# Kernel tuning notes

Measured on AMD Instinct MI355X. Metric: run time of the kernel, lower is better.

Reference implementation:

```python
import jax, jax.numpy as jnp
import numpy as np
import math, itertools

DIM = 384; KEY_DIM = 16; HEADS = 8; ATTN_RATIO = 4; RES = 28
RES2 = math.ceil(RES / 2)            # 14
NH_KD = KEY_DIM * HEADS              # 128
D = ATTN_RATIO * KEY_DIM             # 64
DH = D * HEADS                       # 512
N = RES * RES                        # 784
N2 = RES2 * RES2                     # 196
OUT_DIM = DIM
SCALE = KEY_DIM ** -0.5
BATCH = 64


def build_bias_idxs():
    stride = math.ceil(RES / RES2)
    offsets = {}
    idxs = []
    for p1 in itertools.product(range(RES2), repeat=2):
        for p2 in itertools.product(range(RES), repeat=2):
            off = (abs(p1[0] * stride - p2[0]), abs(p1[1] * stride - p2[1]))
            if off not in offsets:
                offsets[off] = len(offsets)
            idxs.append(offsets[off])
    return np.asarray(idxs, dtype=np.int32), len(offsets)


def dwconv(x, w, b, stride):
    # depthwise 3x3, padding 1; x: (B,C,H,W), w: (C,1,3,3)
    y = jax.lax.conv_general_dilated(
        x, w, (stride, stride), ((1, 1), (1, 1)),
        dimension_numbers=("NCHW", "OIHW", "NCHW"),
        feature_group_count=x.shape[1])
    return y + b[None, :, None, None]


def conv1x1(x, w, b):
    return jnp.einsum("bchw,oc->bohw", x, w) + b[None, :, None, None]


def bn(x, s, o):
    # inference-mode BatchNorm folded to per-channel scale/offset
    return x * s[None, :, None, None] + o[None, :, None, None]


def setup_inputs() -> dict:
    key = jax.random.key(0)
    ks = jax.random.split(key, 25)
    def rn(k, shape, sc=0.05):
        return jax.random.normal(k, shape, jnp.float32) * sc
    idxs, n_off = build_bias_idxs()
    return dict(
        x=jax.random.normal(ks[0], (BATCH, DIM, RES, RES), jnp.float32),
        ql_w=rn(ks[1], (DIM, 1, 3, 3)), ql_b=rn(ks[2], (DIM,)),
        qp_w=rn(ks[3], (NH_KD, DIM)), qp_b=rn(ks[4], (NH_KD,)),
        qp_s=1.0 + rn(ks[5], (NH_KD,)), qp_o=rn(ks[6], (NH_KD,)),
        k_w=rn(ks[7], (NH_KD, DIM)), k_b=rn(ks[8], (NH_KD,)),
        k_s=1.0 + rn(ks[9], (NH_KD,)), k_o=rn(ks[10], (NH_KD,)),
        v_w=rn(ks[11], (DH, DIM)), v_b=rn(ks[12], (DH,)),
        v_s=1.0 + rn(ks[13], (DH,)), v_o=rn(ks[14], (DH,)),
        vl_w=rn(ks[15], (DH, 1, 3, 3)), vl_b=rn(ks[16], (DH,)),
        vl_s=1.0 + rn(ks[17], (DH,)), vl_o=rn(ks[18], (DH,)),
        p_w=rn(ks[19], (OUT_DIM, DH)), p_b=rn(ks[20], (OUT_DIM,)),
        p_s=1.0 + rn(ks[21], (OUT_DIM,)), p_o=rn(ks[22], (OUT_DIM,)),
        ab=rn(ks[23], (HEADS, n_off)),
        bias_idxs=jnp.asarray(idxs),
    )


def reference(x, ql_w, ql_b, qp_w, qp_b, qp_s, qp_o,
              k_w, k_b, k_s, k_o, v_w, v_b, v_s, v_o,
              vl_w, vl_b, vl_s, vl_o, p_w, p_b, p_s, p_o,
              ab, bias_idxs):
    B = x.shape[0]
    # LGQuery: depthwise stride-2 conv + stride-2 avg-pool(k=1), then 1x1 conv + BN
    local_q = dwconv(x, ql_w, ql_b, 2)
    pool_q = x[:, :, ::2, ::2]               # AvgPool2d(1, 2, 0)
    q = bn(conv1x1(local_q + pool_q, qp_w, qp_b), qp_s, qp_o)
    q = q.reshape(B, HEADS, KEY_DIM, N2).transpose(0, 1, 3, 2)   # (B,H,N2,kd)

    k = bn(conv1x1(x, k_w, k_b), k_s, k_o).reshape(B, HEADS, KEY_DIM, N)  # (B,H,kd,N)

    v = bn(conv1x1(x, v_w, v_b), v_s, v_o)   # (B,DH,RES,RES)
    v_local = bn(dwconv(v, vl_w, vl_b, 2), vl_s, vl_o)           # (B,DH,RES2,RES2)
    v = v.reshape(B, HEADS, D, N).transpose(0, 1, 3, 2)          # (B,H,N,d)

    bias = ab[:, bias_idxs].reshape(HEADS, N2, N)                # gathered rel-pos bias
    attn = jnp.einsum("bhqc,bhck->bhqk", q, k) * SCALE + bias[None]
    attn = jax.nn.softmax(attn, axis=-1)

    out = jnp.einsum("bhqk,bhkd->bhqd", attn, v).transpose(0, 1, 3, 2)
    out = out.reshape(B, DH, RES2, RES2) + v_local
    out = bn(conv1x1(jax.nn.gelu(out, approximate=False), p_w, p_b), p_s, p_o)
    return out
```

## Files before the change

### kernel.cpp

```cpp
#include <hip/hip_runtime.h>
#include <math.h>

#define BATCH   64
#define DIMC    384
#define KEY_DIM 16
#define HEADS   8
#define DD      64
#define DH      512
#define NH_KD   128
#define RES     28
#define RES2    14
#define NN      784
#define NN2     196
#define OUT_DIM 384
#define SCALE   0.25f
#define XPAD    896
#define QPAD    256
#define KPAD    832
#define XSP     796

typedef __attribute__((ext_vector_type(8))) short bf16x8;
typedef __attribute__((ext_vector_type(4))) float f32x4;

#define MFMA32(a, b, c) __builtin_amdgcn_mfma_f32_16x16x32_bf16(a, b, c, 0, 0, 0)
#define SWZ(row, bcol) ((row) * 64 + ((bcol) ^ ((((row) >> 1) & 3) << 4)))

__device__ inline short f2bf(float f) {
    unsigned u = __float_as_uint(f);
    unsigned r = (u + 0x7fff + ((u >> 16) & 1)) >> 16;
    return (short)r;
}
__device__ inline float bf2f(short h) {
    return __uint_as_float(((unsigned)(unsigned short)h) << 16);
}
__device__ __forceinline__ unsigned cvt_pk_bf16(float a, float b) {
    unsigned r;
    asm("v_cvt_pk_bf16_f32 %0, %1, %2" : "=v"(r) : "v"(a), "v"(b));
    return r;
}
__device__ __forceinline__ void gload16(const void* g, void* l) {
    __builtin_amdgcn_global_load_lds((const __attribute__((address_space(1))) void*)g,
                                     (__attribute__((address_space(3))) void*)l, 16, 0, 0);
}

#define O_XT_HI    0u
#define O_QINT_HI  44040192u
#define O_QT       88080384u
#define O_KT       96468992u
#define O_V        123731968u
#define O_VLOCAL   178257920u
#define O_BIASB    203948032u
#define O_W_HI     206557184u
#define O_W_LO     207540224u
#define O_ATTNT    0u
#define O_GT_HI    25690112u

__global__ __launch_bounds__(256)
void xprep_kernel(const float* __restrict__ x, const float* __restrict__ ql_w,
                  const float* __restrict__ ql_b, short* __restrict__ xT,
                  short* __restrict__ qinT) {
    __shared__ short xs[32 * XSP];
    const int cg = blockIdx.x, b = blockIdx.y;
    const int t = threadIdx.x;
    const float* xb = x + ((size_t)b * DIMC + cg * 32) * NN;

    {
        const int c = t >> 3, sub = t & 7;
        const float* xc = xb + (size_t)c * NN;
        short* dst = xs + c * XSP;
        #pragma unroll 5
        for (int p4 = sub; p4 < 196; p4 += 8) {
            float4 v = *(const float4*)(xc + p4 * 4);
            uint2 pk = {cvt_pk_bf16(v.x, v.y), cvt_pk_bf16(v.z, v.w)};
            *(uint2*)(dst + p4 * 4) = pk;
        }
    }
    __syncthreads();

    {
        const int c_l = t & 31;
        const int ng  = t >> 5;
        const short* src = xs + c_l * XSP;
        short* dstb = xT + (size_t)b * XPAD * DIMC + cg * 32 + c_l;
        for (int n = ng; n < NN; n += 8)
            dstb[(size_t)n * DIMC] = src[n];
        for (int n = NN + ng; n < XPAD; n += 8)
            dstb[(size_t)n * DIMC] = 0;
    }

    {
        const int c_l = t & 31;
        const int ng  = t >> 5;
        const int c = cg * 32 + c_l;
        const short* xc = xs + c_l * XSP;
        const float* w = ql_w + c * 9;
        const float w0 = w[0], w1 = w[1], w2 = w[2], w3 = w[3], w4 = w[4],
                    w5 = w[5], w6 = w[6], w7 = w[7], w8 = w[8];
        const float bias = ql_b[c];
        short* qdst = qinT + (size_t)b * QPAD * DIMC + c;
        for (int n2 = ng; n2 < NN2; n2 += 8) {
            int i = n2 / RES2, j = n2 % RES2;
            int r0 = 2 * i - 1, c0 = 2 * j - 1;
            float acc = bias;
            if (r0 >= 0) {
                if (c0 >= 0)       acc += bf2f(xc[r0 * RES + c0])     * w0;
                                   acc += bf2f(xc[r0 * RES + c0 + 1]) * w1;
                if (c0 + 2 < RES)  acc += bf2f(xc[r0 * RES + c0 + 2]) * w2;
            }
            {
                if (c0 >= 0)       acc += bf2f(xc[(r0 + 1) * RES + c0])     * w3;
                                   acc += bf2f(xc[(r0 + 1) * RES + c0 + 1]) * w4;
                if (c0 + 2 < RES)  acc += bf2f(xc[(r0 + 1) * RES + c0 + 2]) * w5;
            }
            if (r0 + 2 < RES) {
                if (c0 >= 0)       acc += bf2f(xc[(r0 + 2) * RES + c0])     * w6;
                                   acc += bf2f(xc[(r0 + 2) * RES + c0 + 1]) * w7;
                if (c0 + 2 < RES)  acc += bf2f(xc[(r0 + 2) * RES + c0 + 2]) * w8;
            }
            acc += bf2f(xc[(2 * i) * RES + 2 * j]);
            qdst[(size_t)n2 * DIMC] = f2bf(acc);
        }
        for (int n2 = NN2 + ng; n2 < QPAD; n2 += 8)
            qdst[(size_t)n2 * DIMC] = 0;
    }
}

__global__ void wsplit_kernel(const float* __restrict__ w0, const float* __restrict__ w1,
                              const float* __restrict__ w2, const float* __restrict__ w3,
                              short* __restrict__ hi, short* __restrict__ lo) {
    int i = blockIdx.x * 256 + threadIdx.x;
    if (i >= 491520) return;
    const float* src; int j = i;
    if (j < 49152) src = w0;
    else if (j < 98304) { src = w1; j -= 49152; }
    else if (j < 294912) { src = w2; j -= 98304; }
    else { src = w3; j -= 294912; }
    float v = src[j];
    short h = f2bf(v);
    hi[i] = h;
    lo[i] = f2bf(v - bf2f(h));
}

template<bool WLO, bool SWAP>
__global__ __launch_bounds__(256)
void gemm_split_kernel(const short* __restrict__ wgt_hi, const short* __restrict__ wgt_lo,
                       const short* __restrict__ act,
                       const float* __restrict__ bias, const float* __restrict__ s,
                       const float* __restrict__ off,
                       float* __restrict__ out_f, short* __restrict__ out_b,
                       int mode, int C, int Nn, int Npad, int NPADo, float pscale,
                       int NXn, int NYo, int O) {
    constexpr int NT = 2 + (WLO ? 1 : 0);
    constexpr int STRIDE = NT * 8192;
    constexpr int OFF_A = 0, OFF_B = 8192, OFF_WL = 16384;
    __shared__ __align__(1024) char LDS[2 * STRIDE];

    const int bid = blockIdx.x;
    const int xcd = bid & 7;
    const int g   = bid >> 3;
    const int ot  = g % NYo;
    const int pp  = (g / NYo) * 8 + xcd;
    const int nt  = pp % NXn;
    const int b   = pp / NXn;
    const int n0 = nt * 128, o0 = ot * 128;

    const int t = threadIdx.x;
    const int lane = t & 63, wid = t >> 6;
    const int wm = wid & 1, wn = wid >> 1;
    const int lr = lane & 15, kg = lane >> 4;

    const short* Ahi = SWAP ? act : wgt_hi;
    const short* Bhi = SWAP ? wgt_hi : act;

    f32x4 acc[4][4];
    #pragma unroll
    for (int m = 0; m < 4; ++m)
        #pragma unroll
        for (int n = 0; n < 4; ++n)
            acc[m][n] = (f32x4){0.f, 0.f, 0.f, 0.f};

    const int ccol = (lane & 3) * 16;
    const int r0   = wid * 32 + (lane >> 2);

    auto STAGE = [&](int buf, int k0) {
        char* base = LDS + buf * STRIDE;
        #pragma unroll
        for (int c = 0; c < 2; ++c) {
            int r = r0 + c * 16;
            int bcs = ccol ^ (((r >> 1) & 3) << 4);
            size_t aRow = SWAP ? ((size_t)b * Npad + n0 + r) : (size_t)(o0 + r);
            size_t bRow = SWAP ? (size_t)(o0 + r) : ((size_t)b * Npad + n0 + r);
            char* ldsc = base + wid * 2048 + c * 1024;
            gload16((const char*)Ahi + (aRow * C + k0) * 2 + bcs, ldsc + OFF_A);
            gload16((const char*)Bhi + (bRow * C + k0) * 2 + bcs, ldsc + OFF_B);
            if constexpr (WLO)
                gload16((const char*)wgt_lo + ((size_t)(o0 + r) * C + k0) * 2 + bcs, ldsc + OFF_WL);
        }
    };

    STAGE(0, 0);
    int cur = 0;
    __syncthreads();

    for (int k0 = 0;; k0 += 32) {
        const bool hasNext = (k0 + 32 < C);
        if (hasNext) STAGE(cur ^ 1, k0 + 32);

        char* cb = LDS + cur * STRIDE;
        bf16x8 ah[4], wlm[4];
        #pragma unroll
        for (int m = 0; m < 4; ++m) {
            int row = wm * 64 + m * 16 + lr;
            ah[m] = *(const bf16x8*)(cb + OFF_A + SWZ(row, kg * 16));
            if constexpr (WLO) if (!SWAP) wlm[m] = *(const bf16x8*)(cb + OFF_WL + SWZ(row, kg * 16));
        }
        #pragma unroll
        for (int nf = 0; nf < 4; ++nf) {
            int row = wn * 64 + nf * 16 + lr;
            bf16x8 bh = *(const bf16x8*)(cb + OFF_B + SWZ(row, kg * 16));
            bf16x8 blw;
            if constexpr (WLO) if (SWAP) blw = *(const bf16x8*)(cb + OFF_WL + SWZ(row, kg * 16));
            #pragma unroll
            for (int m = 0; m < 4; ++m) {
                acc[m][nf] = MFMA32(ah[m], bh, acc[m][nf]);
                if constexpr (WLO) {
                    if (SWAP) acc[m][nf] = MFMA32(ah[m], blw, acc[m][nf]);
                    else      acc[m][nf] = MFMA32(wlm[m], bh, acc[m][nf]);
                }
            }
        }
        if (!hasNext) break;
        __syncthreads();
        cur ^= 1;
    }

    if (mode == 2) {
        #pragma unroll
        for (int m = 0; m < 4; ++m) {
            #pragma unroll
            for (int nf = 0; nf < 4; ++nf) {
                int col = n0 + wn * 64 + nf * 16 + lr;
                if (col >= NPADo) continue;
                int hh = (o0 + wm * 64 + m * 16) >> 4;
                bool nok = (col < Nn);
                float v[4];
                #pragma unroll
                for (int r = 0; r < 4; ++r) {
                    int row = o0 + wm * 64 + m * 16 + kg * 4 + r;
                    float a = s[row];
                    v[r] = nok ? (acc[m][nf][r] * a + (bias[row] * a + off[row])) * pscale : 0.f;
                }
                unsigned h01 = cvt_pk_bf16(v[0], v[1]);
                unsigned h23 = cvt_pk_bf16(v[2], v[3]);
                float l0 = v[0] - __uint_as_float(h01 << 16);
                float l1 = v[1] - __uint_as_float(h01 & 0xffff0000u);
                float l2 = v[2] - __uint_as_float(h23 << 16);
                float l3 = v[3] - __uint_as_float(h23 & 0xffff0000u);
                uint2 hst = {h01, h23};
                uint2 lst = {cvt_pk_bf16(l0, l1), cvt_pk_bf16(l2, l3)};
                size_t base = ((size_t)(b * 8 + hh) * NPADo + col) * 32 + kg * 4;
                *(uint2*)(out_b + base)      = hst;
                *(uint2*)(out_b + base + 16) = lst;
            }
        }
    } else {
        #pragma unroll
        for (int nf = 0; nf < 4; ++nf) {
            int col_d = o0 + wn * 64 + nf * 16 + lr;
            float a = s[col_d];
            float badd = bias[col_d] * a + off[col_d];
            #pragma unroll
            for (int m = 0; m < 4; ++m) {
                int rown = n0 + wm * 64 + m * 16 + kg * 4;
                float v0 = acc[m][nf][0] * a + badd;
                float v1 = acc[m][nf][1] * a + badd;
                float v2 = acc[m][nf][2] * a + badd;
                float v3 = acc[m][nf][3] * a + badd;
                if (mode == 0) {
                    if (rown < Nn) {
                        float4 vv = {v0, v1, v2, v3};
                        *(float4*)(out_f + ((size_t)b * O + col_d) * Nn + rown) = vv;
                    }
                } else {
                    if (rown + 3 < NPADo) {
                        uint2 st = {cvt_pk_bf16(v0, v1), cvt_pk_bf16(v2, v3)};
                        *(uint2*)(out_b + ((size_t)b * O + col_d) * NPADo + rown) = st;
                    }
                }
            }
        }
    }
}

__global__ void vlocal_kernel(const short* __restrict__ v,
                              const float* __restrict__ vl_w, const float* __restrict__ vl_b,
                              const float* __restrict__ vl_s, const float* __restrict__ vl_o,
                              float* __restrict__ vlocal) {
    int c = blockIdx.x, b = blockIdx.y, n2 = threadIdx.x;
    if (n2 >= NN2) return;
    int i = n2 / RES2, j = n2 % RES2;
    const size_t base = ((size_t)b * DH + c) * KPAD;
    const float* w = vl_w + c * 9;
    float acc = vl_b[c];
    #pragma unroll
    for (int di = 0; di < 3; ++di) {
        int r = 2 * i + di - 1;
        if (r < 0 || r >= RES) continue;
        #pragma unroll
        for (int dj = 0; dj < 3; ++dj) {
            int cc = 2 * j + dj - 1;
            if (cc < 0 || cc >= RES) continue;
            acc += bf2f(v[base + r * RES + cc]) * w[di * 3 + dj];
        }
    }
    vlocal[((size_t)b * DH + c) * NN2 + n2] = acc * vl_s[c] + vl_o[c];
}

__global__ void biasB_expand_kernel(const float* __restrict__ ab, const int* __restrict__ bidx,
                                    short* __restrict__ biasB, int n_off) {
    int i = blockIdx.x * 256 + threadIdx.x;
    int h = blockIdx.y;
    if (i >= NN2 * KPAD) return;
    int q = i / KPAD, key = i - q * KPAD;
    short v = 0;
    if (key < NN) v = f2bf(ab[h * n_off + bidx[q * NN + key]]);
    biasB[(size_t)h * NN2 * KPAD + i] = v;
}

__global__ __launch_bounds__(512, 4)
void attn_mfma9_kernel(const short* __restrict__ QT, const short* __restrict__ KT,
                       const short* __restrict__ V, const short* __restrict__ biasB,
                       float* __restrict__ outT) {
    __shared__ __align__(1024) char LDS[2 * 12288 + 8 * 4096];

    const int t = threadIdx.x;
    const int bid = blockIdx.x;
    const int h = bid & 7;
    const int b = bid >> 3;

    const int lane = t & 63, wid = t >> 6;
    const int lr = lane & 15, kg = lane >> 4;
    const int wq0 = wid * 32;

    bf16x8 qb1[2], qb2[2];
    const short* bb[2];
    #pragma unroll
    for (int qf = 0; qf < 2; ++qf) {
        int qg = wq0 + qf * 16 + lr;
        const short* qrow = QT + ((size_t)(b * 8 + h) * QPAD + qg) * 32;
        qb1[qf] = *(const bf16x8*)(qrow + (kg & 1) * 8);
        qb2[qf] = (bf16x8){0, 0, 0, 0, 0, 0, 0, 0};
        if (kg < 2) qb2[qf] = *(const bf16x8*)(qrow + 16 + kg * 8);
        int qs = (qg < NN2) ? qg : (NN2 - 1);
        bb[qf] = biasB + ((size_t)h * NN2 + qs) * KPAD;
    }

    const short* kbase = KT + (size_t)(b * 8 + h) * KPAD * 32;
    const short* vbase = V + ((size_t)b * DH + h * DD) * KPAD;

    f32x4 acc[2][4];
    #pragma unroll
    for (int qf = 0; qf < 2; ++qf)
        #pragma unroll
        for (int nt = 0; nt < 4; ++nt)
            acc[qf][nt] = (f32x4){0.f, 0.f, 0.f, 0.f};
    float sacc[2] = {0.f, 0.f};
    char* PsW = LDS + 24576 + wid * 4096;
    const int swz = (lr & 7) << 4;

    auto STAGE = [&](int buf, int tile) {
        const int k0 = tile * 64;
        char* base = LDS + buf * 12288;
        #pragma unroll
        for (int ci = 0; ci < 2; ++ci) {
            if (ci == 1 && wid >= 4) continue;
            int chunk = (ci == 0) ? wid : wid + 8;
            if (chunk < 4) {
                int row = chunk * 16 + (lane >> 2);
                int pcol = (lane & 3) ^ ((row >> 1) & 3);
                gload16((const char*)(kbase + (size_t)(k0 + row) * 32) + pcol * 16,
                        base + chunk * 1024);
            } else {
                int vrow = (chunk - 4) * 8 + (lane >> 3);
                int pcol = (lane & 7) ^ (vrow & 7);
                gload16((const char*)(vbase + (size_t)vrow * KPAD + k0) + pcol * 16,
                        base + 4096 + (chunk - 4) * 1024);
            }
        }
    };

    auto COMPUTE = [&](int buf, int tile) {
        const int k0 = tile * 64;
        char* cb = LDS + buf * 12288;
        short4 b4[2][4];
        #pragma unroll
        for (int qf = 0; qf < 2; ++qf)
            #pragma unroll
            for (int nt = 0; nt < 4; ++nt)
                b4[qf][nt] = *(const short4*)(bb[qf] + k0 + nt * 16 + kg * 4);

        #pragma unroll
        for (int qf = 0; qf < 2; ++qf) {
            f32x4 sc[4];
            __builtin_amdgcn_s_setprio(1);
            #pragma unroll
            for (int nt = 0; nt < 4; ++nt) {
                int row = nt * 16 + lr;
                bf16x8 ka = *(const bf16x8*)(cb + row * 64 + ((kg ^ ((row >> 1) & 3)) * 16));
                sc[nt] = (f32x4){0.f, 0.f, 0.f, 0.f};
                sc[nt] = MFMA32(ka, qb1[qf], sc[nt]);
                sc[nt] = MFMA32(ka, qb2[qf], sc[nt]);
            }
            __builtin_amdgcn_s_setprio(0);

            char* Psw = PsW + qf * 2048;
            #pragma unroll
            for (int nt = 0; nt < 4; ++nt) {
                int keyb = k0 + nt * 16 + kg * 4;
                bool kvalid = keyb < NN;
                float pv[4];
                #pragma unroll
                for (int r = 0; r < 4; ++r) {
                    float sv = sc[nt][r] + bf2f(((const short*)&b4[qf][nt])[r]);
                    pv[r] = kvalid ? __expf(sv) : 0.f;
                    sacc[qf] += pv[r];
                }
                uint2 pk2 = {cvt_pk_bf16(pv[0], pv[1]), cvt_pk_bf16(pv[2], pv[3])};
                *(uint2*)(Psw + lr * 128 + ((nt * 32 + kg * 8) ^ swz)) = pk2;
            }
        }

        #pragma unroll
        for (int ks = 0; ks < 2; ++ks) {
            bf16x8 vf[4];
            #pragma unroll
            for (int nt = 0; nt < 4; ++nt) {
                int row = nt * 16 + lr;
                int pk_ = ks * 4 + kg;
                vf[nt] = *(const bf16x8*)(cb + 4096 + row * 128 + ((pk_ ^ (row & 7)) * 16));
            }
            #pragma unroll
            for (int qf = 0; qf < 2; ++qf) {
                bf16x8 pa = *(const bf16x8*)(PsW + qf * 2048 + lr * 128
                                             + ((ks * 64 + kg * 16) ^ swz));
                __builtin_amdgcn_s_setprio(1);
                #pragma unroll
                for (int nt = 0; nt < 4; ++nt)
                    acc[qf][nt] = MFMA32(pa, vf[nt], acc[qf][nt]);
                __builtin_amdgcn_s_setprio(0);
            }
        }
    };

    STAGE(0, 0);
    int cur = 0;
    __syncthreads();
    #pragma unroll 1
    for (int tile = 0; tile < 13; ++tile) {
        if (tile + 1 < 13) STAGE(cur ^ 1, tile + 1);
        COMPUTE(cur, tile);
        __syncthreads();
        cur ^= 1;
    }

    #pragma unroll
    for (int qf = 0; qf < 2; ++qf) {
        float sv = sacc[qf];
        sv += __shfl_xor(sv, 16, 64);
        sv += __shfl_xor(sv, 32, 64);
        #pragma unroll
        for (int r = 0; r < 4; ++r) {
            int qrow_ = wq0 + qf * 16 + kg * 4 + r;
            if (qrow_ >= NN2) continue;
            float inv = 1.f / __shfl(sv, kg * 4 + r, 64);
            #pragma unroll
            for (int nt = 0; nt < 4; ++nt) {
                int d = nt * 16 + lr;
                outT[((size_t)b * NN2 + qrow_) * DH + h * DD + d] = acc[qf][nt][r] * inv;
            }
        }
    }
}

__global__ void gelu_addT_kernel(const float* __restrict__ aT, const float* __restrict__ vloc,
                                 short* __restrict__ g_hi) {
    __shared__ float tile[32][33];
    int ntb = blockIdx.x * 32, ctb = blockIdx.y * 32, b = blockIdx.z;
    int tn = threadIdx.x & 31, tc4 = threadIdx.x >> 5;
    #pragma unroll
    for (int i = 0; i < 4; ++i) {
        int c = tc4 + i * 8;
        int n = ntb + tn;
        tile[c][tn] = (n < NN2) ? vloc[((size_t)b * DH + ctb + c) * NN2 + n] : 0.f;
    }
    __syncthreads();
    int tc = threadIdx.x & 31, tn4 = threadIdx.x >> 5;
    #pragma unroll
    for (int i = 0; i < 4; ++i) {
        int n = ntb + tn4 + i * 8;
        float g = 0.f;
        if (n < NN2) {
            float sum = aT[((size_t)b * NN2 + n) * DH + ctb + tc] + tile[tc][tn4 + i * 8];
            g = 0.5f * sum * (1.f + erff(sum * 0.70710678118654752440f));
        }
        g_hi[((size_t)b * QPAD + n) * DH + ctb + tc] = f2bf(g);
    }
}

extern "C" void kernel_launch(void* const* d_in, const int* in_sizes, int n_in,
                              void* d_out, int out_size, void* d_ws, size_t ws_size,
                              hipStream_t stream) {
    const float* x     = (const float*)d_in[0];
    const float* ql_w  = (const float*)d_in[1];
    const float* ql_b  = (const float*)d_in[2];
    const float* qp_w  = (const float*)d_in[3];
    const float* qp_b  = (const float*)d_in[4];
    const float* qp_s  = (const float*)d_in[5];
    const float* qp_o  = (const float*)d_in[6];
    const float* k_w   = (const float*)d_in[7];
    const float* k_b   = (const float*)d_in[8];
    const float* k_s   = (const float*)d_in[9];
    const float* k_o   = (const float*)d_in[10];
    const float* v_w   = (const float*)d_in[11];
    const float* v_b   = (const float*)d_in[12];
    const float* v_s   = (const float*)d_in[13];
    const float* v_o   = (const float*)d_in[14];
    const float* vl_w  = (const float*)d_in[15];
    const float* vl_b  = (const float*)d_in[16];
    const float* vl_s  = (const float*)d_in[17];
    const float* vl_o  = (const float*)d_in[18];
    const float* p_w   = (const float*)d_in[19];
    const float* p_b   = (const float*)d_in[20];
    const float* p_s   = (const float*)d_in[21];
    const float* p_o   = (const float*)d_in[22];
    const float* ab    = (const float*)d_in[23];
    const int*   bidx  = (const int*)d_in[24];
    float* out = (float*)d_out;
    int n_off = in_sizes[23] / HEADS;

    char* ws = (char*)d_ws;
    short* qinT_h = (short*)(ws + O_QINT_HI);
    short* xT_h   = (short*)(ws + O_XT_HI);
    short* QT     = (short*)(ws + O_QT);
    short* KT     = (short*)(ws + O_KT);
    short* Vb     = (short*)(ws + O_V);
    float* vlocal = (float*)(ws + O_VLOCAL);
    short* biasB  = (short*)(ws + O_BIASB);
    short* w_h    = (short*)(ws + O_W_HI);
    short* w_l    = (short*)(ws + O_W_LO);
    float* attnT  = (float*)(ws + O_ATTNT);
    short* gT_h   = (short*)(ws + O_GT_HI);

    xprep_kernel<<<dim3(DIMC / 32, BATCH), 256, 0, stream>>>(x, ql_w, ql_b, xT_h, qinT_h);
    wsplit_kernel<<<dim3(1920), 256, 0, stream>>>(qp_w, k_w, v_w, p_w, w_h, w_l);
    gemm_split_kernel<false, false><<<dim3(128), 256, 0, stream>>>(
        w_h + 0, nullptr, qinT_h, qp_b, qp_s, qp_o,
        nullptr, QT, 2, DIMC, NN2, QPAD, QPAD, SCALE, 2, 1, 128);
    gemm_split_kernel<false, false><<<dim3(448), 256, 0, stream>>>(
        w_h + 49152, nullptr, xT_h, k_b, k_s, k_o,
        nullptr, KT, 2, DIMC, NN, XPAD, KPAD, 1.0f, 7, 1, 128);
    gemm_split_kernel<false, true><<<dim3(1792), 256, 0, stream>>>(
        w_h + 98304, nullptr, xT_h, v_b, v_s, v_o,
        nullptr, Vb, 1, DIMC, NN, XPAD, KPAD, 1.0f, 7, 4, 512);
    vlocal_kernel<<<dim3(DH, BATCH), 256, 0, stream>>>(Vb, vl_w, vl_b, vl_s, vl_o, vlocal);
    biasB_expand_kernel<<<dim3((NN2 * KPAD + 255) / 256, HEADS), 256, 0, stream>>>(ab, bidx, biasB, n_off);
    attn_mfma9_kernel<<<dim3(HEADS * BATCH), 512, 0, stream>>>(QT, KT, Vb, biasB, attnT);
    gelu_addT_kernel<<<dim3(QPAD / 32, DH / 32, BATCH), 256, 0, stream>>>(attnT, vlocal, gT_h);
    gemm_split_kernel<true, true><<<dim3(384), 256, 0, stream>>>(
        w_h + 294912, w_l + 294912, gT_h, p_b, p_s, p_o,
        out, nullptr, 0, DH, NN2, QPAD, 0, 1.0f, 2, 3, 384);
}
```

Baseline: 274.3 us.

## Fuse vlocal add and GELU into attention epilogue, use exp2 softmax

Attention now adds the transposed v_local and applies exact GELU in its epilogue, writing bf16 directly for the projection GEMM. This removes the separate gelu_addT kernel and the fp32 attention intermediate. vlocal is rewritten to produce a token-major layout via an LDS transpose. log2(e) is folded into the Q scale and bias so the softmax uses exp2f. The final projection drops the hi/lo weight split, trading some precision for fewer MFMA passes.

```diff
diff --git a/kernel.cpp b/kernel.cpp
--- a/kernel.cpp
+++ b/kernel.cpp
@@ -14,6 +14,7 @@
 #define NN2     196
 #define OUT_DIM 384
 #define SCALE   0.25f
+#define LOG2E   1.44269504088896340736f
 #define XPAD    896
 #define QPAD    256
 #define KPAD    832
@@ -48,11 +49,10 @@
 #define O_QT       88080384u
 #define O_KT       96468992u
 #define O_V        123731968u
-#define O_VLOCAL   178257920u
+#define O_VLT      178257920u
 #define O_BIASB    203948032u
 #define O_W_HI     206557184u
 #define O_W_LO     207540224u
-#define O_ATTNT    0u
 #define O_GT_HI    25690112u
 
 __global__ __launch_bounds__(256)
@@ -292,28 +292,50 @@
     }
 }
 
-__global__ void vlocal_kernel(const short* __restrict__ v,
-                              const float* __restrict__ vl_w, const float* __restrict__ vl_b,
-                              const float* __restrict__ vl_s, const float* __restrict__ vl_o,
-                              float* __restrict__ vlocal) {
-    int c = blockIdx.x, b = blockIdx.y, n2 = threadIdx.x;
-    if (n2 >= NN2) return;
-    int i = n2 / RES2, j = n2 % RES2;
-    const size_t base = ((size_t)b * DH + c) * KPAD;
-    const float* w = vl_w + c * 9;
-    float acc = vl_b[c];
-    #pragma unroll
-    for (int di = 0; di < 3; ++di) {
-        int r = 2 * i + di - 1;
-        if (r < 0 || r >= RES) continue;
-        #pragma unroll
-        for (int dj = 0; dj < 3; ++dj) {
-            int cc = 2 * j + dj - 1;
-            if (cc < 0 || cc >= RES) continue;
-            acc += bf2f(v[base + r * RES + cc]) * w[di * 3 + dj];
-        }
-    }
-    vlocal[((size_t)b * DH + c) * NN2 + n2] = acc * vl_s[c] + vl_o[c];
+__global__ __launch_bounds__(256)
+void vlocalT_kernel(const short* __restrict__ v,
+                    const float* __restrict__ vl_w, const float* __restrict__ vl_b,
+                    const float* __restrict__ vl_s, const float* __restrict__ vl_o,
+                    float* __restrict__ vlT) {
+    __shared__ float tile[32][201];
+    const int cg = blockIdx.x, b = blockIdx.y;
+    const int t = threadIdx.x;
+    {
+        const int c_l = t >> 3, nsub = t & 7;
+        const int c = cg * 32 + c_l;
+        const size_t base = ((size_t)b * DH + c) * KPAD;
+        const float* w = vl_w + c * 9;
+        const float w0 = w[0], w1 = w[1], w2 = w[2], w3 = w[3], w4 = w[4],
+                    w5 = w[5], w6 = w[6], w7 = w[7], w8 = w[8];
+        const float bias = vl_b[c], sc = vl_s[c], of = vl_o[c];
+        for (int n2 = nsub; n2 < NN2; n2 += 8) {
+            int i = n2 / RES2, j = n2 % RES2;
+            int r0 = 2 * i - 1, c0 = 2 * j - 1;
+            float acc = bias;
+            if (r0 >= 0) {
+                if (c0 >= 0)       acc += bf2f(v[base + r0 * RES + c0])     * w0;
+                                   acc += bf2f(v[base + r0 * RES + c0 + 1]) * w1;
+                if (c0 + 2 < RES)  acc += bf2f(v[base + r0 * RES + c0 + 2]) * w2;
+            }
+            {
+                if (c0 >= 0)       acc += bf2f(v[base + (r0 + 1) * RES + c0])     * w3;
+                                   acc += bf2f(v[base + (r0 + 1) * RES + c0 + 1]) * w4;
+                if (c0 + 2 < RES)  acc += bf2f(v[base + (r0 + 1) * RES + c0 + 2]) * w5;
+            }
+            if (r0 + 2 < RES) {
+                if (c0 >= 0)       acc += bf2f(v[base + (r0 + 2) * RES + c0])     * w6;
+                                   acc += bf2f(v[base + (r0 + 2) * RES + c0 + 1]) * w7;
+                if (c0 + 2 < RES)  acc += bf2f(v[base + (r0 + 2) * RES + c0 + 2]) * w8;
+            }
+            tile[c_l][n2] = acc * sc + of;
+        }
+    }
+    __syncthreads();
+    {
+        const int c_l = t & 31, ng = t >> 5;
+        for (int n2 = ng; n2 < NN2; n2 += 8)
+            vlT[((size_t)b * NN2 + n2) * DH + cg * 32 + c_l] = tile[c_l][n2];
+    }
 }
 
 __global__ void biasB_expand_kernel(const float* __restrict__ ab, const int* __restrict__ bidx,
@@ -323,14 +345,14 @@
     if (i >= NN2 * KPAD) return;
     int q = i / KPAD, key = i - q * KPAD;
     short v = 0;
-    if (key < NN) v = f2bf(ab[h * n_off + bidx[q * NN + key]]);
+    if (key < NN) v = f2bf(ab[h * n_off + bidx[q * NN + key]] * LOG2E);
     biasB[(size_t)h * NN2 * KPAD + i] = v;
 }
 
 __global__ __launch_bounds__(512, 4)
-void attn_mfma9_kernel(const short* __restrict__ QT, const short* __restrict__ KT,
-                       const short* __restrict__ V, const short* __restrict__ biasB,
-                       float* __restrict__ outT) {
+void attn_mfma10_kernel(const short* __restrict__ QT, const short* __restrict__ KT,
+                        const short* __restrict__ V, const short* __restrict__ biasB,
+                        const float* __restrict__ vlT, short* __restrict__ gT) {
     __shared__ __align__(1024) char LDS[2 * 12288 + 8 * 4096];
 
     const int t = threadIdx.x;
@@ -422,7 +444,7 @@
                 #pragma unroll
                 for (int r = 0; r < 4; ++r) {
                     float sv = sc[nt][r] + bf2f(((const short*)&b4[qf][nt])[r]);
-                    pv[r] = kvalid ? __expf(sv) : 0.f;
+                    pv[r] = kvalid ? exp2f(sv) : 0.f;
                     sacc[qf] += pv[r];
                 }
                 uint2 pk2 = {cvt_pk_bf16(pv[0], pv[1]), cvt_pk_bf16(pv[2], pv[3])};
@@ -473,37 +495,16 @@
             int qrow_ = wq0 + qf * 16 + kg * 4 + r;
             if (qrow_ >= NN2) continue;
             float inv = 1.f / __shfl(sv, kg * 4 + r, 64);
+            const float* vrow = vlT + ((size_t)b * NN2 + qrow_) * DH + h * DD;
+            short* grow = gT + ((size_t)b * QPAD + qrow_) * DH + h * DD;
             #pragma unroll
             for (int nt = 0; nt < 4; ++nt) {
                 int d = nt * 16 + lr;
-                outT[((size_t)b * NN2 + qrow_) * DH + h * DD + d] = acc[qf][nt][r] * inv;
-            }
-        }
-    }
-}
-
-__global__ void gelu_addT_kernel(const float* __restrict__ aT, const float* __restrict__ vloc,
-                                 short* __restrict__ g_hi) {
-    __shared__ float tile[32][33];
-    int ntb = blockIdx.x * 32, ctb = blockIdx.y * 32, b = blockIdx.z;
-    int tn = threadIdx.x & 31, tc4 = threadIdx.x >> 5;
-    #pragma unroll
-    for (int i = 0; i < 4; ++i) {
-        int c = tc4 + i * 8;
-        int n = ntb + tn;
-        tile[c][tn] = (n < NN2) ? vloc[((size_t)b * DH + ctb + c) * NN2 + n] : 0.f;
-    }
-    __syncthreads();
-    int tc = threadIdx.x & 31, tn4 = threadIdx.x >> 5;
-    #pragma unroll
-    for (int i = 0; i < 4; ++i) {
-        int n = ntb + tn4 + i * 8;
-        float g = 0.f;
-        if (n < NN2) {
-            float sum = aT[((size_t)b * NN2 + n) * DH + ctb + tc] + tile[tc][tn4 + i * 8];
-            g = 0.5f * sum * (1.f + erff(sum * 0.70710678118654752440f));
-        }
-        g_hi[((size_t)b * QPAD + n) * DH + ctb + tc] = f2bf(g);
+                float s_ = acc[qf][nt][r] * inv + vrow[d];
+                float g = 0.5f * s_ * (1.f + erff(s_ * 0.70710678118654752440f));
+                grow[d] = f2bf(g);
+            }
+        }
     }
 }
 
@@ -544,29 +545,27 @@
     short* QT     = (short*)(ws + O_QT);
     short* KT     = (short*)(ws + O_KT);
     short* Vb     = (short*)(ws + O_V);
-    float* vlocal = (float*)(ws + O_VLOCAL);
+    float* vlT    = (float*)(ws + O_VLT);
     short* biasB  = (short*)(ws + O_BIASB);
     short* w_h    = (short*)(ws + O_W_HI);
     short* w_l    = (short*)(ws + O_W_LO);
-    float* attnT  = (float*)(ws + O_ATTNT);
     short* gT_h   = (short*)(ws + O_GT_HI);
 
     xprep_kernel<<<dim3(DIMC / 32, BATCH), 256, 0, stream>>>(x, ql_w, ql_b, xT_h, qinT_h);
     wsplit_kernel<<<dim3(1920), 256, 0, stream>>>(qp_w, k_w, v_w, p_w, w_h, w_l);
     gemm_split_kernel<false, false><<<dim3(128), 256, 0, stream>>>(
         w_h + 0, nullptr, qinT_h, qp_b, qp_s, qp_o,
-        nullptr, QT, 2, DIMC, NN2, QPAD, QPAD, SCALE, 2, 1, 128);
+        nullptr, QT, 2, DIMC, NN2, QPAD, QPAD, SCALE * LOG2E, 2, 1, 128);
     gemm_split_kernel<false, false><<<dim3(448), 256, 0, stream>>>(
         w_h + 49152, nullptr, xT_h, k_b, k_s, k_o,
         nullptr, KT, 2, DIMC, NN, XPAD, KPAD, 1.0f, 7, 1, 128);
     gemm_split_kernel<false, true><<<dim3(1792), 256, 0, stream>>>(
         w_h + 98304, nullptr, xT_h, v_b, v_s, v_o,
         nullptr, Vb, 1, DIMC, NN, XPAD, KPAD, 1.0f, 7, 4, 512);
-    vlocal_kernel<<<dim3(DH, BATCH), 256, 0, stream>>>(Vb, vl_w, vl_b, vl_s, vl_o, vlocal);
+    vlocalT_kernel<<<dim3(DH / 32, BATCH), 256, 0, stream>>>(Vb, vl_w, vl_b, vl_s, vl_o, vlT);
     biasB_expand_kernel<<<dim3((NN2 * KPAD + 255) / 256, HEADS), 256, 0, stream>>>(ab, bidx, biasB, n_off);
-    attn_mfma9_kernel<<<dim3(HEADS * BATCH), 512, 0, stream>>>(QT, KT, Vb, biasB, attnT);
-    gelu_addT_kernel<<<dim3(QPAD / 32, DH / 32, BATCH), 256, 0, stream>>>(attnT, vlocal, gT_h);
-    gemm_split_kernel<true, true><<<dim3(384), 256, 0, stream>>>(
-        w_h + 294912, w_l + 294912, gT_h, p_b, p_s, p_o,
+    attn_mfma10_kernel<<<dim3(HEADS * BATCH), 512, 0, stream>>>(QT, KT, Vb, biasB, vlT, gT_h);
+    gemm_split_kernel<false, true><<<dim3(384), 256, 0, stream>>>(
+        w_h + 294912, nullptr, gT_h, p_b, p_s, p_o,
         out, nullptr, 0, DH, NN2, QPAD, 0, 1.0f, 2, 3, 384);
 }
```

Result: no change. 279.2 us (+1.8%).
